# Performance work log

Hardware: AMD Instinct MI355X
Metric: run time of the kernel (lower is better)

The kernel has to match this reference:

```python
import jax, jax.numpy as jnp
import numpy as np

NQ, M, ND, N, H, DIM = 32, 32, 200, 160, 768, 128
TEMP = 0.1      # log_softmax temperature
TAU = 0.5       # gumbel-softmax temperature
NEG = -10000.0


def _l2norm(x):
    # F.normalize(p=2, dim=-1) with eps clamp
    n = jnp.maximum(jnp.linalg.norm(x, axis=-1, keepdims=True), 1e-12)
    return x / n


def setup_inputs() -> dict:
    key = jax.random.key(0)
    k1, k2, k3, k4, k5, k6 = jax.random.split(key, 6)
    Q = jax.random.normal(k1, (NQ, M, H), dtype=jnp.float32)
    D = jax.random.normal(k2, (ND, N, H), dtype=jnp.float32)
    q_mask = jax.random.randint(k3, (NQ, M), 0, 2).astype(jnp.float32)
    d_mask = jax.random.randint(k4, (ND, N), 0, 2).astype(jnp.float32)
    # pre-sampled Gumbel(0,1) noise for gumbel_softmax (fixed for determinism)
    u = jax.random.uniform(k5, (NQ, ND, M, N), dtype=jnp.float32,
                           minval=1e-6, maxval=1.0 - 1e-6)
    gumbel_noise = -jnp.log(-jnp.log(u))
    # proj_linear: Linear(768, dim, bias=False)
    W_proj = jax.random.normal(k6, (H, DIM), dtype=jnp.float32) / np.sqrt(H)
    return {"Q": Q, "D": D, "q_mask": q_mask, "d_mask": d_mask,
            "gumbel_noise": gumbel_noise, "W_proj": W_proj}


def reference(Q, D, q_mask, d_mask, gumbel_noise, W_proj):
    # project + L2-normalize token embeddings
    Qp = _l2norm(Q @ W_proj)            # [q, m, dim]
    Dp = _l2norm(D @ W_proj)            # [d, n, dim]

    # pairwise token similarities: [q, d, m, n]
    sim = jnp.einsum('qmh,dnh->qdmn', Qp, Dp)

    dm = d_mask[None, :, None, :]       # [1, d, 1, n]
    sim_masked = sim * dm + (1.0 - dm) * NEG

    logits = jax.nn.log_softmax(sim_masked / TEMP, axis=-1)

    # gumbel_softmax(tau=0.5, hard=True) with straight-through
    y_soft = jax.nn.softmax((logits + gumbel_noise) / TAU, axis=-1)
    idx = jnp.argmax(y_soft, axis=-1)
    y_hard = jax.nn.one_hot(idx, N, dtype=y_soft.dtype)
    y = jax.lax.stop_gradient(y_hard - y_soft) + y_soft

    # select doc token per query token, mask query tokens, sum -> [q, d]
    scores = (y * sim_masked).sum(-1)          # [q, d, m]
    scores = scores * q_mask[:, None, :]
    return scores.sum(-1)                      # [q, d]
```

## Files before the change

### kernel.cpp

```cpp
#include <hip/hip_runtime.h>
#include <math.h>

#define NQ_   32
#define M_    32
#define ND_   200
#define N_    160
#define H_    768
#define DIM_  128
#define DROWS_ (ND_ * N_)
#define QROWS_ (NQ_ * M_)
#define TROWS_ (DROWS_ + QROWS_)

__device__ __forceinline__ void gl_lds16(const float* g, float* l) {
    __builtin_amdgcn_global_load_lds(
        (const __attribute__((address_space(1))) unsigned int*)g,
        (__attribute__((address_space(3))) unsigned int*)l, 16, 0, 0);
}

__global__ __launch_bounds__(128) void proj_kernel(
    const float* __restrict__ Dmat, const float* __restrict__ Qmat,
    const float* __restrict__ W, float* __restrict__ DpT,
    float* __restrict__ QpT)
{
    __shared__ float Xt[16][32];
    __shared__ float Ws[16][128];
    const int tid = threadIdx.x;
    const int rb  = blockIdx.x * 32;
    const int cg  = tid & 15;
    const int rg  = tid >> 4;

    float acc[4][8];
#pragma unroll
    for (int i = 0; i < 4; ++i)
#pragma unroll
        for (int j = 0; j < 8; ++j) acc[i][j] = 0.0f;

    for (int kc = 0; kc < H_; kc += 16) {
        {
            int row = tid >> 2, c4 = tid & 3;
            int r = rb + row;
            const float* xr = (r < DROWS_) ? (Dmat + (size_t)r * H_)
                                           : (Qmat + (size_t)(r - DROWS_) * H_);
            float4 v = *reinterpret_cast<const float4*>(xr + kc + c4 * 4);
            Xt[c4*4+0][row] = v.x;
            Xt[c4*4+1][row] = v.y;
            Xt[c4*4+2][row] = v.z;
            Xt[c4*4+3][row] = v.w;
        }
#pragma unroll
        for (int it = 0; it < 4; ++it) {
            int f = tid + it * 128;
            int wr = f >> 5, wc = f & 31;
            *reinterpret_cast<float4*>(&Ws[wr][wc*4]) =
                *reinterpret_cast<const float4*>(&W[(size_t)(kc + wr) * DIM_ + wc * 4]);
        }
        __syncthreads();
#pragma unroll
        for (int k = 0; k < 16; ++k) {
            float a[4], b[8];
            *reinterpret_cast<float4*>(&a[0]) = *reinterpret_cast<const float4*>(&Xt[k][rg*4]);
            *reinterpret_cast<float4*>(&b[0]) = *reinterpret_cast<const float4*>(&Ws[k][cg*8]);
            *reinterpret_cast<float4*>(&b[4]) = *reinterpret_cast<const float4*>(&Ws[k][cg*8+4]);
#pragma unroll
            for (int i = 0; i < 4; ++i)
#pragma unroll
                for (int j = 0; j < 8; ++j)
                    acc[i][j] = fmaf(a[i], b[j], acc[i][j]);
        }
        __syncthreads();
    }

#pragma unroll
    for (int i = 0; i < 4; ++i) {
        int r = rb + rg * 4 + i;
        float ss = 0.0f;
#pragma unroll
        for (int j = 0; j < 8; ++j) ss = __fadd_rn(ss, __fmul_rn(acc[i][j], acc[i][j]));
        ss = __fadd_rn(ss, __shfl_xor(ss, 1));
        ss = __fadd_rn(ss, __shfl_xor(ss, 2));
        ss = __fadd_rn(ss, __shfl_xor(ss, 4));
        ss = __fadd_rn(ss, __shfl_xor(ss, 8));
        float nrm = fmaxf(sqrtf(ss), 1e-12f);
        if (r < DROWS_) {
            int dd = r / 160, n = r - dd * 160;
            float* o = DpT + (size_t)dd * (DIM_ * N_) + n;
#pragma unroll
            for (int j = 0; j < 8; ++j)
                o[(size_t)(cg*8 + j) * N_] = acc[i][j] / nrm;
        } else {
            int rq = r - DROWS_;
            int qq = rq >> 5, m = rq & 31;
            float* o = QpT + (size_t)qq * (DIM_ * M_) + m;
#pragma unroll
            for (int j = 0; j < 8; ++j)
                o[(size_t)(cg*8 + j) * M_] = acc[i][j] / nrm;
        }
    }
}

__global__ __launch_bounds__(64) void score_kernel(
    const float* __restrict__ QpT, const float* __restrict__ DpT,
    const float* __restrict__ qmask, const float* __restrict__ dmask,
    const float* __restrict__ gum, float* __restrict__ out)
{
    __shared__ float Qt[8][32];
    __shared__ float Dt[8][160];
    const int lane = threadIdx.x;
    const int mg   = lane >> 4;
    const int ng   = lane & 15;
    const int q    = blockIdx.x & 31;
    const int d    = blockIdx.x >> 5;

    const float* Qb = QpT + (size_t)q * (DIM_ * M_);
    const float* Db = DpT + (size_t)d * (DIM_ * N_);

    float acc[8][10];
#pragma unroll
    for (int i = 0; i < 8; ++i)
#pragma unroll
        for (int j = 0; j < 10; ++j) acc[i][j] = 0.0f;

    for (int kc = 0; kc < DIM_; kc += 8) {
        gl_lds16(Qb + kc * M_ + lane * 4, &Qt[0][0]);
#pragma unroll
        for (int c = 0; c < 5; ++c)
            gl_lds16(Db + kc * N_ + c * 256 + lane * 4, &Dt[0][0] + c * 256);
        __syncthreads();
#pragma unroll
        for (int k = 0; k < 8; ++k) {
            float a[8], b[10];
            *reinterpret_cast<float4*>(&a[0]) = *reinterpret_cast<const float4*>(&Qt[k][mg*8]);
            *reinterpret_cast<float4*>(&a[4]) = *reinterpret_cast<const float4*>(&Qt[k][mg*8+4]);
            const float* bp = &Dt[k][ng*10];
#pragma unroll
            for (int j2 = 0; j2 < 5; ++j2)
                *reinterpret_cast<float2*>(&b[j2*2]) = *reinterpret_cast<const float2*>(&bp[j2*2]);
#pragma unroll
            for (int i = 0; i < 8; ++i)
#pragma unroll
                for (int j = 0; j < 10; ++j)
                    acc[i][j] = fmaf(a[i], b[j], acc[i][j]);
        }
        __syncthreads();
    }

    float dmv[10];
#pragma unroll
    for (int j = 0; j < 10; ++j)
        dmv[j] = dmask[(size_t)d * N_ + ng*10 + j];

    const float* gq = gum + ((size_t)q * ND_ + d) * ((size_t)M_ * N_);

    float partial = 0.0f;
#pragma unroll
    for (int i = 0; i < 8; ++i) {
        const int m = mg*8 + i;
        float x[10];
        float mx = -3.402823466e38f;
#pragma unroll
        for (int j = 0; j < 10; ++j) {
            float sm = (dmv[j] != 0.0f) ? acc[i][j] : -10000.0f;
            x[j] = sm / 0.1f;
            mx = fmaxf(mx, x[j]);
        }
        mx = fmaxf(mx, __shfl_xor(mx, 1));
        mx = fmaxf(mx, __shfl_xor(mx, 2));
        mx = fmaxf(mx, __shfl_xor(mx, 4));
        mx = fmaxf(mx, __shfl_xor(mx, 8));

        float se = 0.0f;
#pragma unroll
        for (int j = 0; j < 10; ++j) se = __fadd_rn(se, expf(x[j] - mx));
        se = __fadd_rn(se, __shfl_xor(se, 1));
        se = __fadd_rn(se, __shfl_xor(se, 2));
        se = __fadd_rn(se, __shfl_xor(se, 4));
        se = __fadd_rn(se, __shfl_xor(se, 8));
        const float lse = logf(se);

        float g[10];
        const float2* gp = reinterpret_cast<const float2*>(&gq[(size_t)m * N_ + ng*10]);
#pragma unroll
        for (int j2 = 0; j2 < 5; ++j2)
            *reinterpret_cast<float2*>(&g[j2*2]) = gp[j2];

        float z[10];
        float mz = -3.402823466e38f;
#pragma unroll
        for (int j = 0; j < 10; ++j) {
            z[j] = ((x[j] - mx - lse) + g[j]) / 0.5f;
            mz = fmaxf(mz, z[j]);
        }
        mz = fmaxf(mz, __shfl_xor(mz, 1));
        mz = fmaxf(mz, __shfl_xor(mz, 2));
        mz = fmaxf(mz, __shfl_xor(mz, 4));
        mz = fmaxf(mz, __shfl_xor(mz, 8));

        float e2[10];
        float s2 = 0.0f;
#pragma unroll
        for (int j = 0; j < 10; ++j) { e2[j] = expf(z[j] - mz); s2 = __fadd_rn(s2, e2[j]); }
        s2 = __fadd_rn(s2, __shfl_xor(s2, 1));
        s2 = __fadd_rn(s2, __shfl_xor(s2, 2));
        s2 = __fadd_rn(s2, __shfl_xor(s2, 4));
        s2 = __fadd_rn(s2, __shfl_xor(s2, 8));

        float besty = -1.0f; int bestn = 0x7fffffff; float bests = 0.0f;
#pragma unroll
        for (int j = 0; j < 10; ++j) {
            float y = e2[j] / s2;
            if (y > besty) {
                besty = y;
                bestn = ng*10 + j;
                bests = (dmv[j] != 0.0f) ? acc[i][j] : -10000.0f;
            }
        }
#pragma unroll
        for (int dl = 1; dl < 16; dl <<= 1) {
            float oy = __shfl_xor(besty, dl);
            int   on = __shfl_xor(bestn, dl);
            float os = __shfl_xor(bests, dl);
            if (oy > besty || (oy == besty && on < bestn)) {
                besty = oy; bestn = on; bests = os;
            }
        }
        const float qmv = qmask[q * M_ + m];
        if (ng == 0) partial = __fadd_rn(partial, __fmul_rn(bests, qmv));
    }
    partial = __fadd_rn(partial, __shfl_xor(partial, 16));
    partial = __fadd_rn(partial, __shfl_xor(partial, 32));
    if (lane == 0) out[(size_t)q * ND_ + d] = partial;
}

extern "C" void kernel_launch(void* const* d_in, const int* in_sizes, int n_in,
                              void* d_out, int out_size, void* d_ws, size_t ws_size,
                              hipStream_t stream)
{
    const float* Q   = (const float*)d_in[0];
    const float* D   = (const float*)d_in[1];
    const float* qm  = (const float*)d_in[2];
    const float* dm  = (const float*)d_in[3];
    const float* gum = (const float*)d_in[4];
    const float* W   = (const float*)d_in[5];
    float* out = (float*)d_out;

    float* QpT = (float*)d_ws;
    float* DpT = QpT + (size_t)QROWS_ * DIM_;

    proj_kernel<<<dim3(TROWS_ / 32), dim3(128), 0, stream>>>(D, Q, W, DpT, QpT);
    score_kernel<<<dim3(NQ_ * ND_), dim3(64), 0, stream>>>(QpT, DpT, qm, dm, gum, out);
}
```

Measured before the change: 503.9 us.

## Enlarge register tiles in projection and score kernels to raise data reuse

The projection kernel now uses 64-thread blocks, each computing a 48-row by 128-column tile with 12x8 accumulators per lane. W is staged through direct global-to-LDS loads and results are written as paired float2 stores. The score kernel now handles 2 queries by 2 docs per 128-thread block with 16x10 accumulators per lane, so each D tile in LDS is shared by two query waves. The aim is fewer LDS and global loads per FMA and fewer launched blocks, at the cost of much higher register pressure and the occupancy loss that comes with it.

```diff
diff --git a/kernel.cpp b/kernel.cpp
--- a/kernel.cpp
+++ b/kernel.cpp
@@ -17,52 +17,57 @@
         (__attribute__((address_space(3))) unsigned int*)l, 16, 0, 0);
 }
 
-__global__ __launch_bounds__(128) void proj_kernel(
+__global__ __launch_bounds__(64, 3) void proj_kernel(
     const float* __restrict__ Dmat, const float* __restrict__ Qmat,
     const float* __restrict__ W, float* __restrict__ DpT,
     float* __restrict__ QpT)
 {
-    __shared__ float Xt[16][32];
-    __shared__ float Ws[16][128];
-    const int tid = threadIdx.x;
-    const int rb  = blockIdx.x * 32;
-    const int cg  = tid & 15;
-    const int rg  = tid >> 4;
-
-    float acc[4][8];
-#pragma unroll
-    for (int i = 0; i < 4; ++i)
+    __shared__ float Xt[8][48];
+    __shared__ float Ws[8][128];
+    const int lane  = threadIdx.x;
+    const int rg    = lane & 3;
+    const int cg    = lane >> 2;
+    const int rbase = blockIdx.x * 48;
+
+    float acc[12][8];
+#pragma unroll
+    for (int i = 0; i < 12; ++i)
 #pragma unroll
         for (int j = 0; j < 8; ++j) acc[i][j] = 0.0f;
 
-    for (int kc = 0; kc < H_; kc += 16) {
-        {
-            int row = tid >> 2, c4 = tid & 3;
-            int r = rb + row;
-            const float* xr = (r < DROWS_) ? (Dmat + (size_t)r * H_)
-                                           : (Qmat + (size_t)(r - DROWS_) * H_);
-            float4 v = *reinterpret_cast<const float4*>(xr + kc + c4 * 4);
-            Xt[c4*4+0][row] = v.x;
-            Xt[c4*4+1][row] = v.y;
-            Xt[c4*4+2][row] = v.z;
-            Xt[c4*4+3][row] = v.w;
-        }
-#pragma unroll
-        for (int it = 0; it < 4; ++it) {
-            int f = tid + it * 128;
-            int wr = f >> 5, wc = f & 31;
-            *reinterpret_cast<float4*>(&Ws[wr][wc*4]) =
-                *reinterpret_cast<const float4*>(&W[(size_t)(kc + wr) * DIM_ + wc * 4]);
-        }
-        __syncthreads();
-#pragma unroll
-        for (int k = 0; k < 16; ++k) {
-            float a[4], b[8];
-            *reinterpret_cast<float4*>(&a[0]) = *reinterpret_cast<const float4*>(&Xt[k][rg*4]);
-            *reinterpret_cast<float4*>(&b[0]) = *reinterpret_cast<const float4*>(&Ws[k][cg*8]);
-            *reinterpret_cast<float4*>(&b[4]) = *reinterpret_cast<const float4*>(&Ws[k][cg*8+4]);
-#pragma unroll
-            for (int i = 0; i < 4; ++i)
+    for (int kc = 0; kc < H_; kc += 8) {
+#pragma unroll
+        for (int it = 0; it < 2; ++it) {
+            int idx = it * 64 + lane;
+            if (idx < 96) {
+                int row = idx >> 1, kh = idx & 1;
+                int r = rbase + row;
+                const float* xr = (r < DROWS_) ? (Dmat + (size_t)r * H_)
+                                               : (Qmat + (size_t)(r - DROWS_) * H_);
+                float4 v = *reinterpret_cast<const float4*>(xr + kc + kh * 4);
+                Xt[kh*4+0][row] = v.x;
+                Xt[kh*4+1][row] = v.y;
+                Xt[kh*4+2][row] = v.z;
+                Xt[kh*4+3][row] = v.w;
+            }
+        }
+#pragma unroll
+        for (int c = 0; c < 4; ++c)
+            gl_lds16(W + (size_t)kc * DIM_ + c * 256 + lane * 4, &Ws[0][0] + c * 256);
+        __syncthreads();
+#pragma unroll
+        for (int k = 0; k < 8; ++k) {
+            float a[12], b[8];
+#pragma unroll
+            for (int ii = 0; ii < 6; ++ii)
+                *reinterpret_cast<float2*>(&a[ii*2]) =
+                    *reinterpret_cast<const float2*>(&Xt[k][rg*2 + 8*ii]);
+#pragma unroll
+            for (int jj = 0; jj < 4; ++jj)
+                *reinterpret_cast<float2*>(&b[jj*2]) =
+                    *reinterpret_cast<const float2*>(&Ws[k][cg*2 + 32*jj]);
+#pragma unroll
+            for (int i = 0; i < 12; ++i)
 #pragma unroll
                 for (int j = 0; j < 8; ++j)
                     acc[i][j] = fmaf(a[i], b[j], acc[i][j]);
@@ -71,72 +76,96 @@
     }
 
 #pragma unroll
-    for (int i = 0; i < 4; ++i) {
-        int r = rb + rg * 4 + i;
-        float ss = 0.0f;
-#pragma unroll
-        for (int j = 0; j < 8; ++j) ss = __fadd_rn(ss, __fmul_rn(acc[i][j], acc[i][j]));
-        ss = __fadd_rn(ss, __shfl_xor(ss, 1));
-        ss = __fadd_rn(ss, __shfl_xor(ss, 2));
-        ss = __fadd_rn(ss, __shfl_xor(ss, 4));
-        ss = __fadd_rn(ss, __shfl_xor(ss, 8));
-        float nrm = fmaxf(sqrtf(ss), 1e-12f);
-        if (r < DROWS_) {
-            int dd = r / 160, n = r - dd * 160;
-            float* o = DpT + (size_t)dd * (DIM_ * N_) + n;
+    for (int ii = 0; ii < 6; ++ii) {
+        float nr[2];
+#pragma unroll
+        for (int p = 0; p < 2; ++p) {
+            float ss = 0.0f;
 #pragma unroll
             for (int j = 0; j < 8; ++j)
-                o[(size_t)(cg*8 + j) * N_] = acc[i][j] / nrm;
+                ss = __fadd_rn(ss, __fmul_rn(acc[ii*2+p][j], acc[ii*2+p][j]));
+            ss = __fadd_rn(ss, __shfl_xor(ss, 4));
+            ss = __fadd_rn(ss, __shfl_xor(ss, 8));
+            ss = __fadd_rn(ss, __shfl_xor(ss, 16));
+            ss = __fadd_rn(ss, __shfl_xor(ss, 32));
+            nr[p] = fmaxf(sqrtf(ss), 1e-12f);
+        }
+        const int r0 = rbase + rg*2 + 8*ii;
+        float* base; int stride;
+        if (r0 < DROWS_) {
+            int dd = r0 / 160, n = r0 - dd * 160;
+            base = DpT + (size_t)dd * (DIM_ * N_) + n; stride = N_;
         } else {
-            int rq = r - DROWS_;
+            int rq = r0 - DROWS_;
             int qq = rq >> 5, m = rq & 31;
-            float* o = QpT + (size_t)qq * (DIM_ * M_) + m;
-#pragma unroll
-            for (int j = 0; j < 8; ++j)
-                o[(size_t)(cg*8 + j) * M_] = acc[i][j] / nrm;
-        }
-    }
-}
-
-__global__ __launch_bounds__(64) void score_kernel(
+            base = QpT + (size_t)qq * (DIM_ * M_) + m; stride = M_;
+        }
+#pragma unroll
+        for (int jj = 0; jj < 4; ++jj)
+#pragma unroll
+            for (int pc = 0; pc < 2; ++pc) {
+                int c = cg*2 + 32*jj + pc;
+                float2 v;
+                v.x = acc[ii*2+0][jj*2+pc] / nr[0];
+                v.y = acc[ii*2+1][jj*2+pc] / nr[1];
+                *reinterpret_cast<float2*>(base + (size_t)c * stride) = v;
+            }
+    }
+}
+
+__global__ __launch_bounds__(128, 2) void score_kernel(
     const float* __restrict__ QpT, const float* __restrict__ DpT,
     const float* __restrict__ qmask, const float* __restrict__ dmask,
     const float* __restrict__ gum, float* __restrict__ out)
 {
-    __shared__ float Qt[8][32];
-    __shared__ float Dt[8][160];
-    const int lane = threadIdx.x;
-    const int mg   = lane >> 4;
-    const int ng   = lane & 15;
-    const int q    = blockIdx.x & 31;
-    const int d    = blockIdx.x >> 5;
-
-    const float* Qb = QpT + (size_t)q * (DIM_ * M_);
-    const float* Db = DpT + (size_t)d * (DIM_ * N_);
-
-    float acc[8][10];
-#pragma unroll
-    for (int i = 0; i < 8; ++i)
+    __shared__ float Dt[2][8][160];
+    __shared__ float Qt[2][8][32];
+    const int tid  = threadIdx.x;
+    const int w    = tid >> 6;
+    const int lane = tid & 63;
+    const int mg   = lane >> 5;
+    const int ng   = lane & 31;
+    const int dpr  = ng >> 4;
+    const int nn   = ng & 15;
+    const int qb   = blockIdx.x & 15;
+    const int dp   = blockIdx.x >> 4;
+    const int q    = qb * 2 + w;
+    const int d    = dp * 2 + dpr;
+
+    const float* Qb  = QpT + (size_t)q * (DIM_ * M_);
+    const float* Db0 = DpT + (size_t)(dp * 2) * (DIM_ * N_);
+
+    float acc[16][10];
+#pragma unroll
+    for (int i = 0; i < 16; ++i)
 #pragma unroll
         for (int j = 0; j < 10; ++j) acc[i][j] = 0.0f;
 
     for (int kc = 0; kc < DIM_; kc += 8) {
-        gl_lds16(Qb + kc * M_ + lane * 4, &Qt[0][0]);
-#pragma unroll
-        for (int c = 0; c < 5; ++c)
-            gl_lds16(Db + kc * N_ + c * 256 + lane * 4, &Dt[0][0] + c * 256);
+        gl_lds16(Qb + kc * M_ + lane * 4, &Qt[w][0][0]);
+#pragma unroll
+        for (int it = 0; it < 5; ++it) {
+            int s  = it * 2 + w;
+            int sd = (s >= 5) ? 1 : 0;
+            int so = s - sd * 5;
+            gl_lds16(Db0 + (size_t)sd * (DIM_ * N_) + kc * N_ + so * 256 + lane * 4,
+                     &Dt[0][0][0] + s * 256);
+        }
         __syncthreads();
 #pragma unroll
         for (int k = 0; k < 8; ++k) {
-            float a[8], b[10];
-            *reinterpret_cast<float4*>(&a[0]) = *reinterpret_cast<const float4*>(&Qt[k][mg*8]);
-            *reinterpret_cast<float4*>(&a[4]) = *reinterpret_cast<const float4*>(&Qt[k][mg*8+4]);
-            const float* bp = &Dt[k][ng*10];
+            float a[16], b[10];
+#pragma unroll
+            for (int c = 0; c < 4; ++c)
+                *reinterpret_cast<float4*>(&a[c*4]) =
+                    *reinterpret_cast<const float4*>(&Qt[w][k][mg*16 + c*4]);
+            const float* bp = &Dt[dpr][k][nn*10];
 #pragma unroll
             for (int j2 = 0; j2 < 5; ++j2)
-                *reinterpret_cast<float2*>(&b[j2*2]) = *reinterpret_cast<const float2*>(&bp[j2*2]);
-#pragma unroll
-            for (int i = 0; i < 8; ++i)
+                *reinterpret_cast<float2*>(&b[j2*2]) =
+                    *reinterpret_cast<const float2*>(&bp[j2*2]);
+#pragma unroll
+            for (int i = 0; i < 16; ++i)
 #pragma unroll
                 for (int j = 0; j < 10; ++j)
                     acc[i][j] = fmaf(a[i], b[j], acc[i][j]);
@@ -147,14 +176,14 @@
     float dmv[10];
 #pragma unroll
     for (int j = 0; j < 10; ++j)
-        dmv[j] = dmask[(size_t)d * N_ + ng*10 + j];
+        dmv[j] = dmask[(size_t)d * N_ + nn*10 + j];
 
     const float* gq = gum + ((size_t)q * ND_ + d) * ((size_t)M_ * N_);
 
-    float partial = 0.0f;
-#pragma unroll
-    for (int i = 0; i < 8; ++i) {
-        const int m = mg*8 + i;
+    float p0 = 0.0f, p1 = 0.0f;
+#pragma unroll
+    for (int i = 0; i < 16; ++i) {
+        const int m = mg*16 + i;
         float x[10];
         float mx = -3.402823466e38f;
 #pragma unroll
@@ -178,7 +207,7 @@
         const float lse = logf(se);
 
         float g[10];
-        const float2* gp = reinterpret_cast<const float2*>(&gq[(size_t)m * N_ + ng*10]);
+        const float2* gp = reinterpret_cast<const float2*>(&gq[(size_t)m * N_ + nn*10]);
 #pragma unroll
         for (int j2 = 0; j2 < 5; ++j2)
             *reinterpret_cast<float2*>(&g[j2*2]) = gp[j2];
@@ -210,7 +239,7 @@
             float y = e2[j] / s2;
             if (y > besty) {
                 besty = y;
-                bestn = ng*10 + j;
+                bestn = nn*10 + j;
                 bests = (dmv[j] != 0.0f) ? acc[i][j] : -10000.0f;
             }
         }
@@ -224,11 +253,14 @@
             }
         }
         const float qmv = qmask[q * M_ + m];
-        if (ng == 0) partial = __fadd_rn(partial, __fmul_rn(bests, qmv));
-    }
-    partial = __fadd_rn(partial, __shfl_xor(partial, 16));
+        float contrib = __fmul_rn(bests, qmv);
+        if (i < 8) p0 = __fadd_rn(p0, contrib);
+        else       p1 = __fadd_rn(p1, contrib);
+    }
+    float partial = __fadd_rn(p0, p1);
     partial = __fadd_rn(partial, __shfl_xor(partial, 32));
-    if (lane == 0) out[(size_t)q * ND_ + d] = partial;
+    if (nn == 0 && mg == 0)
+        out[(size_t)q * ND_ + d] = partial;
 }
 
 extern "C" void kernel_launch(void* const* d_in, const int* in_sizes, int n_in,
@@ -246,6 +278,6 @@
     float* QpT = (float*)d_ws;
     float* DpT = QpT + (size_t)QROWS_ * DIM_;
 
-    proj_kernel<<<dim3(TROWS_ / 32), dim3(128), 0, stream>>>(D, Q, W, DpT, QpT);
-    score_kernel<<<dim3(NQ_ * ND_), dim3(64), 0, stream>>>(QpT, DpT, qm, dm, gum, out);
-}
+    proj_kernel<<<dim3(TROWS_ / 48), dim3(64), 0, stream>>>(D, Q, W, DpT, QpT);
+    score_kernel<<<dim3((NQ_ / 2) * (ND_ / 2)), dim3(128), 0, stream>>>(QpT, DpT, qm, dm, gum, out);
+}
```

Result: slower. 988.7 us (+96.2%).
